# Performance work log

Measured on AMD Instinct MI355X. Metric: run time of the kernel, lower is better.

Reference implementation:

```python
import jax, jax.numpy as jnp
import numpy as np

N_NODES = 100000
N_RAND_EDGES = 6400000
N_EDGES = N_RAND_EDGES + N_NODES  # + self loops (dgl.add_self_loop)
IN_FEATS, HIDDEN, N_CLASSES = 16, 8, 2


def setup_inputs() -> dict:
    key = jax.random.key(0)
    ks = jax.random.split(key, 8)
    x = jax.random.normal(ks[0], (N_NODES, IN_FEATS), dtype=jnp.float32)
    src_r = jax.random.randint(ks[1], (N_RAND_EDGES,), 0, N_NODES, dtype=jnp.int32)
    dst_r = jax.random.randint(ks[2], (N_RAND_EDGES,), 0, N_NODES, dtype=jnp.int32)
    loop = jnp.arange(N_NODES, dtype=jnp.int32)
    src = jnp.concatenate([src_r, loop])
    dst = jnp.concatenate([dst_r, loop])
    timestamp = jax.random.uniform(ks[3], (N_EDGES,), dtype=jnp.float32)
    W1 = jax.random.normal(ks[4], (IN_FEATS, HIDDEN), dtype=jnp.float32) / np.sqrt(IN_FEATS)
    b1 = jnp.zeros((HIDDEN,), dtype=jnp.float32)
    W2 = jax.random.normal(ks[5], (HIDDEN, N_CLASSES), dtype=jnp.float32) / np.sqrt(HIDDEN)
    b2 = jnp.zeros((N_CLASSES,), dtype=jnp.float32)
    return {"x": x, "src": src, "dst": dst, "timestamp": timestamp,
            "W1": W1, "b1": b1, "W2": W2, "b2": b2}


def _gcn_layer(h, src, dst, ts, W, b):
    # message: u_mul_e -> src feature scaled by scalar edge weight  [E, F]
    msg = h[src] * ts[:, None]
    # reduce: max over incoming edges per destination node
    agg = jax.ops.segment_max(msg, dst, num_segments=N_NODES)
    # DGL fills nodes with no in-edges with 0 (self-loops make this rare)
    agg = jnp.where(jnp.isfinite(agg), agg, 0.0)
    return agg @ W + b


def reference(x, src, dst, timestamp, W1, b1, W2, b2):
    h = _gcn_layer(x, src, dst, timestamp, W1, b1)
    h = jax.nn.relu(h)
    # dropout(p=0.5, train=False) -> identity in eval mode
    out = _gcn_layer(h, src, dst, timestamp, W2, b2)
    return out
```

## Files before the change

kernel.cpp:

```cpp
#include <hip/hip_runtime.h>
#include <hip/hip_bf16.h>

#define N_NODES 100000
#define N_EDGES 6500000
#define IN_FEATS 16
#define HIDDEN 8
#define N_CLASSES 2
#define BK 196
#define NBK 512
#define EPB 8192
#define CAP 16384

__device__ __forceinline__ unsigned f2key(float f) {
    int i = __float_as_int(f);
    return (unsigned)(i ^ ((i >> 31) | 0x80000000));
}
__device__ __forceinline__ float key2f(unsigned u) {
    int i = (u & 0x80000000u) ? (int)(u ^ 0x80000000u) : (int)(~u);
    return __int_as_float(i);
}
__device__ __forceinline__ unsigned pack_bf16(float f0, float f1) {
    unsigned u0 = __float_as_uint(f0), u1 = __float_as_uint(f1);
    u0 = (u0 + 0x7FFFu + ((u0 >> 16) & 1u)) >> 16;
    u1 = (u1 + 0x7FFFu + ((u1 >> 16) & 1u)) >> 16;
    return u0 | (u1 << 16);
}

__global__ void init_cursor(unsigned* __restrict__ cursor) {
    int t = threadIdx.x;
    if (t < NBK) cursor[t] = (unsigned)t * CAP;
}

__global__ __launch_bounds__(1024, 8) void binfill(
    const float* __restrict__ x, const int* __restrict__ src,
    const int* __restrict__ dst, const float* __restrict__ ts,
    unsigned* __restrict__ cursor, uint2* __restrict__ binned,
    unsigned* __restrict__ xb) {
    __shared__ uint2 stage[EPB];
    __shared__ unsigned lcnt[NBK];
    __shared__ unsigned lstart[NBK + 1];
    __shared__ unsigned shiftv[NBK];
    __shared__ unsigned waveTot[8], waveBase[8];
    int t = threadIdx.x;
    if (t < NBK) lcnt[t] = 0u;
    for (int i = blockIdx.x * 1024 + t; i < N_NODES * IN_FEATS / 2; i += gridDim.x * 1024)
        xb[i] = pack_bf16(x[2 * i], x[2 * i + 1]);
    __syncthreads();
    int base = blockIdx.x * EPB;
    unsigned pk[8];
#pragma unroll
    for (int k = 0; k < 8; ++k) {
        int e = base + k * 1024 + t;
        pk[k] = 0xFFFFFFFFu;
        if (e < N_EDGES) {
            unsigned d = (unsigned)dst[e];
            unsigned b = d / BK;
            unsigned slot = atomicAdd(&lcnt[b], 1u);
            pk[k] = ((d - b * BK) << 22) | (b << 13) | slot;
        }
    }
    __syncthreads();
    unsigned c = (t < NBK) ? lcnt[t] : 0u;
    unsigned inc = c;
    int lane = t & 63;
#pragma unroll
    for (int d = 1; d < 64; d <<= 1) {
        unsigned v = __shfl_up(inc, d, 64);
        if (lane >= d) inc += v;
    }
    if (t < NBK && lane == 63) waveTot[t >> 6] = inc;
    __syncthreads();
    if (t == 0) {
        unsigned acc = 0;
#pragma unroll
        for (int w = 0; w < 8; ++w) { waveBase[w] = acc; acc += waveTot[w]; }
    }
    __syncthreads();
    if (t < NBK) {
        unsigned excl = waveBase[t >> 6] + inc - c;
        lstart[t] = excl;
        unsigned gb = atomicAdd(&cursor[t], c);
        shiftv[t] = gb - excl;
        if (t == NBK - 1) lstart[NBK] = excl + c;
    }
    __syncthreads();
#pragma unroll
    for (int k = 0; k < 8; ++k) {
        if (pk[k] != 0xFFFFFFFFu) {
            int e = base + k * 1024 + t;
            unsigned b = (pk[k] >> 13) & 511u;
            unsigned pos = lstart[b] + (pk[k] & 8191u);
            unsigned sv = (unsigned)__builtin_nontemporal_load(&src[e]);
            float tv = __builtin_nontemporal_load(&ts[e]);
            stage[pos] = make_uint2(sv | ((pk[k] >> 22) << 17), __float_as_uint(tv));
        }
    }
    __syncthreads();
    unsigned total = lstart[NBK];
#pragma unroll
    for (int j = 0; j < 8; ++j) {
        unsigned i = (unsigned)t + j * 1024u;
        if (i < total) {
            unsigned lo = 0, hi = NBK - 1;
            while (lo < hi) {
                unsigned mid = (lo + hi + 1) >> 1;
                if (lstart[mid] <= i) lo = mid; else hi = mid - 1;
            }
            uint2 v = stage[i];
            __builtin_nontemporal_store(((unsigned long long)v.y << 32) | v.x,
                                        (unsigned long long*)&binned[i + shiftv[lo]]);
        }
    }
}

__device__ __forceinline__ void agg16(unsigned* row, uint4 a, uint4 b, float tv) {
    const unsigned* pa = (const unsigned*)&a;
    const unsigned* pb = (const unsigned*)&b;
#pragma unroll
    for (int w = 0; w < 8; ++w) {
        unsigned u = (w < 4) ? pa[w] : pb[w - 4];
        atomicMax(row + 2 * w,     f2key(__uint_as_float(u << 16) * tv));
        atomicMax(row + 2 * w + 1, f2key(__uint_as_float(u & 0xFFFF0000u) * tv));
    }
}

__global__ __launch_bounds__(1024, 8) void layer1(
    const unsigned* __restrict__ cursor, const uint2* __restrict__ binned,
    const uint4* __restrict__ xb, const float* __restrict__ W1,
    const float* __restrict__ b1, uint4* __restrict__ hb) {
    __shared__ unsigned tile[BK * 17];
    __shared__ float sW[IN_FEATS * HIDDEN];
    __shared__ float sb[HIDDEN];
    int t = threadIdx.x;
    if (t < IN_FEATS * HIDDEN) sW[t] = W1[t];
    if (t < HIDDEN) sb[t] = b1[t];
    for (int i = t; i < BK * 17; i += 1024) tile[i] = 0u;
    __syncthreads();
    unsigned e0 = blockIdx.x * CAP;
    unsigned e1 = cursor[blockIdx.x];
    unsigned e = e0 + t;
    for (; e + 2048 < e1; e += 3072) {
        unsigned long long r0 = __builtin_nontemporal_load((const unsigned long long*)&binned[e]);
        unsigned long long r1 = __builtin_nontemporal_load((const unsigned long long*)&binned[e + 1024]);
        unsigned long long r2 = __builtin_nontemporal_load((const unsigned long long*)&binned[e + 2048]);
        unsigned s0 = (unsigned)r0 & 0x1FFFFu, d0 = ((unsigned)r0) >> 17;
        unsigned s1 = (unsigned)r1 & 0x1FFFFu, d1 = ((unsigned)r1) >> 17;
        unsigned s2 = (unsigned)r2 & 0x1FFFFu, d2 = ((unsigned)r2) >> 17;
        float t0 = __uint_as_float((unsigned)(r0 >> 32));
        float t1 = __uint_as_float((unsigned)(r1 >> 32));
        float t2 = __uint_as_float((unsigned)(r2 >> 32));
        uint4 a0 = xb[s0 * 2], c0 = xb[s0 * 2 + 1];
        uint4 a1 = xb[s1 * 2], c1 = xb[s1 * 2 + 1];
        uint4 a2 = xb[s2 * 2], c2 = xb[s2 * 2 + 1];
        agg16(tile + d0 * 17, a0, c0, t0);
        agg16(tile + d1 * 17, a1, c1, t1);
        agg16(tile + d2 * 17, a2, c2, t2);
    }
    for (; e < e1; e += 1024) {
        unsigned long long r0 = __builtin_nontemporal_load((const unsigned long long*)&binned[e]);
        unsigned s0 = (unsigned)r0 & 0x1FFFFu, d0 = ((unsigned)r0) >> 17;
        float t0 = __uint_as_float((unsigned)(r0 >> 32));
        uint4 a0 = xb[s0 * 2], c0 = xb[s0 * 2 + 1];
        agg16(tile + d0 * 17, a0, c0, t0);
    }
    __syncthreads();
    int node = blockIdx.x * BK + t;
    if (t < BK && node < N_NODES) {
        float a[IN_FEATS];
#pragma unroll
        for (int f = 0; f < IN_FEATS; ++f) a[f] = key2f(tile[t * 17 + f]);
        float o[HIDDEN];
#pragma unroll
        for (int j = 0; j < HIDDEN; ++j) {
            float sacc = sb[j];
#pragma unroll
            for (int f = 0; f < IN_FEATS; ++f) sacc += a[f] * sW[f * HIDDEN + j];
            o[j] = fmaxf(sacc, 0.f);
        }
        hb[node] = make_uint4(pack_bf16(o[0], o[1]), pack_bf16(o[2], o[3]),
                              pack_bf16(o[4], o[5]), pack_bf16(o[6], o[7]));
    }
}

__device__ __forceinline__ void agg8(unsigned* row, uint4 a, float tv) {
    const unsigned* pa = (const unsigned*)&a;
#pragma unroll
    for (int w = 0; w < 4; ++w) {
        unsigned u = pa[w];
        atomicMax(row + 2 * w,     f2key(__uint_as_float(u << 16) * tv));
        atomicMax(row + 2 * w + 1, f2key(__uint_as_float(u & 0xFFFF0000u) * tv));
    }
}

__global__ __launch_bounds__(1024, 8) void layer2(
    const unsigned* __restrict__ cursor, const uint2* __restrict__ binned,
    const uint4* __restrict__ hb, const float* __restrict__ W2,
    const float* __restrict__ b2, float* __restrict__ out) {
    __shared__ unsigned tile[BK * 9];
    __shared__ float sW[HIDDEN * N_CLASSES];
    __shared__ float sb[N_CLASSES];
    int t = threadIdx.x;
    if (t < HIDDEN * N_CLASSES) sW[t] = W2[t];
    if (t < N_CLASSES) sb[t] = b2[t];
    for (int i = t; i < BK * 9; i += 1024) tile[i] = 0u;
    __syncthreads();
    unsigned e0 = blockIdx.x * CAP;
    unsigned e1 = cursor[blockIdx.x];
    unsigned e = e0 + t;
    for (; e + 3072 < e1; e += 4096) {
        unsigned long long r0 = __builtin_nontemporal_load((const unsigned long long*)&binned[e]);
        unsigned long long r1 = __builtin_nontemporal_load((const unsigned long long*)&binned[e + 1024]);
        unsigned long long r2 = __builtin_nontemporal_load((const unsigned long long*)&binned[e + 2048]);
        unsigned long long r3 = __builtin_nontemporal_load((const unsigned long long*)&binned[e + 3072]);
        unsigned s0 = (unsigned)r0 & 0x1FFFFu, d0 = ((unsigned)r0) >> 17;
        unsigned s1 = (unsigned)r1 & 0x1FFFFu, d1 = ((unsigned)r1) >> 17;
        unsigned s2 = (unsigned)r2 & 0x1FFFFu, d2 = ((unsigned)r2) >> 17;
        unsigned s3 = (unsigned)r3 & 0x1FFFFu, d3 = ((unsigned)r3) >> 17;
        float t0 = __uint_as_float((unsigned)(r0 >> 32));
        float t1 = __uint_as_float((unsigned)(r1 >> 32));
        float t2 = __uint_as_float((unsigned)(r2 >> 32));
        float t3 = __uint_as_float((unsigned)(r3 >> 32));
        uint4 h0 = hb[s0], h1 = hb[s1], h2 = hb[s2], h3 = hb[s3];
        agg8(tile + d0 * 9, h0, t0);
        agg8(tile + d1 * 9, h1, t1);
        agg8(tile + d2 * 9, h2, t2);
        agg8(tile + d3 * 9, h3, t3);
    }
    for (; e < e1; e += 1024) {
        unsigned long long r0 = __builtin_nontemporal_load((const unsigned long long*)&binned[e]);
        unsigned s0 = (unsigned)r0 & 0x1FFFFu, d0 = ((unsigned)r0) >> 17;
        float t0 = __uint_as_float((unsigned)(r0 >> 32));
        agg8(tile + d0 * 9, hb[s0], t0);
    }
    __syncthreads();
    int node = blockIdx.x * BK + t;
    if (t < BK && node < N_NODES) {
        float a[HIDDEN];
#pragma unroll
        for (int f = 0; f < HIDDEN; ++f) a[f] = key2f(tile[t * 9 + f]);
        float o0 = sb[0], o1 = sb[1];
#pragma unroll
        for (int f = 0; f < HIDDEN; ++f) {
            o0 += a[f] * sW[f * N_CLASSES + 0];
            o1 += a[f] * sW[f * N_CLASSES + 1];
        }
        ((float2*)out)[node] = make_float2(o0, o1);
    }
}

__global__ void fb_init_keys(unsigned* __restrict__ k1, unsigned* __restrict__ k2) {
    int i = blockIdx.x * blockDim.x + threadIdx.x;
    for (int idx = i; idx < N_NODES * IN_FEATS; idx += gridDim.x * blockDim.x) k1[idx] = 0u;
    for (int idx = i; idx < N_NODES * HIDDEN; idx += gridDim.x * blockDim.x) k2[idx] = 0u;
}
__global__ void fb_scatter1(const int* __restrict__ src, const int* __restrict__ dst,
                            const float* __restrict__ ts, const float* __restrict__ x,
                            unsigned* __restrict__ agg) {
    int e = blockIdx.x * blockDim.x + threadIdx.x;
    if (e >= N_EDGES) return;
    int s = src[e]; int d = dst[e]; float t = ts[e];
    const float4* xs = (const float4*)(x + (size_t)s * IN_FEATS);
    unsigned* a = agg + (size_t)d * IN_FEATS;
#pragma unroll
    for (int q = 0; q < 4; ++q) {
        float4 v = xs[q];
        atomicMax(a + q * 4 + 0, f2key(v.x * t));
        atomicMax(a + q * 4 + 1, f2key(v.y * t));
        atomicMax(a + q * 4 + 2, f2key(v.z * t));
        atomicMax(a + q * 4 + 3, f2key(v.w * t));
    }
}
__global__ void fb_node1(const unsigned* __restrict__ agg, const float* __restrict__ W1,
                         const float* __restrict__ b1, float* __restrict__ h) {
    int n = blockIdx.x * blockDim.x + threadIdx.x;
    if (n >= N_NODES) return;
    float a[IN_FEATS];
#pragma unroll
    for (int f = 0; f < IN_FEATS; ++f) a[f] = key2f(agg[(size_t)n * IN_FEATS + f]);
#pragma unroll
    for (int j = 0; j < HIDDEN; ++j) {
        float acc = b1[j];
#pragma unroll
        for (int f = 0; f < IN_FEATS; ++f) acc += a[f] * W1[f * HIDDEN + j];
        h[(size_t)n * HIDDEN + j] = acc > 0.f ? acc : 0.f;
    }
}
__global__ void fb_scatter2(const int* __restrict__ src, const int* __restrict__ dst,
                            const float* __restrict__ ts, const float* __restrict__ h,
                            unsigned* __restrict__ agg) {
    int e = blockIdx.x * blockDim.x + threadIdx.x;
    if (e >= N_EDGES) return;
    int s = src[e]; int d = dst[e]; float t = ts[e];
    const float4* hs = (const float4*)(h + (size_t)s * HIDDEN);
    unsigned* a = agg + (size_t)d * HIDDEN;
#pragma unroll
    for (int q = 0; q < 2; ++q) {
        float4 v = hs[q];
        atomicMax(a + q * 4 + 0, f2key(v.x * t));
        atomicMax(a + q * 4 + 1, f2key(v.y * t));
        atomicMax(a + q * 4 + 2, f2key(v.z * t));
        atomicMax(a + q * 4 + 3, f2key(v.w * t));
    }
}
__global__ void fb_node2(const unsigned* __restrict__ agg, const float* __restrict__ W2,
                         const float* __restrict__ b2, float* __restrict__ out) {
    int n = blockIdx.x * blockDim.x + threadIdx.x;
    if (n >= N_NODES) return;
    float a[HIDDEN];
#pragma unroll
    for (int f = 0; f < HIDDEN; ++f) a[f] = key2f(agg[(size_t)n * HIDDEN + f]);
#pragma unroll
    for (int j = 0; j < N_CLASSES; ++j) {
        float acc = b2[j];
#pragma unroll
        for (int f = 0; f < HIDDEN; ++f) acc += a[f] * W2[f * N_CLASSES + j];
        out[(size_t)n * N_CLASSES + j] = acc;
    }
}

extern "C" void kernel_launch(void* const* d_in, const int* in_sizes, int n_in,
                              void* d_out, int out_size, void* d_ws, size_t ws_size,
                              hipStream_t stream) {
    const float* x  = (const float*)d_in[0];
    const int* src  = (const int*)d_in[1];
    const int* dst  = (const int*)d_in[2];
    const float* ts = (const float*)d_in[3];
    const float* W1 = (const float*)d_in[4];
    const float* b1 = (const float*)d_in[5];
    const float* W2 = (const float*)d_in[6];
    const float* b2 = (const float*)d_in[7];
    float* out = (float*)d_out;

    char* ws = (char*)d_ws;
    size_t off = 0;
    auto alloc = [&](size_t bytes) { char* p = ws + off; off += (bytes + 255) & ~(size_t)255; return p; };

    unsigned* cursor = (unsigned*)alloc(NBK * 4);
    uint2*    binned = (uint2*)alloc((size_t)NBK * CAP * 8);
    uint4*    hb     = (uint4*)alloc((size_t)N_NODES * 16);
    unsigned* xb     = (unsigned*)alloc((size_t)N_NODES * IN_FEATS * 2);
    size_t fast_need = off;

    int eblocks = (N_EDGES + EPB - 1) / EPB;

    if (fast_need <= ws_size) {
        init_cursor<<<1, NBK, 0, stream>>>(cursor);
        binfill<<<eblocks, 1024, 0, stream>>>(x, src, dst, ts, cursor, binned, xb);
        layer1<<<NBK, 1024, 0, stream>>>(cursor, binned, (const uint4*)xb, W1, b1, hb);
        layer2<<<NBK, 1024, 0, stream>>>(cursor, binned, hb, W2, b2, out);
    } else {
        unsigned* k1 = (unsigned*)d_ws;
        float* hh    = (float*)(k1 + (size_t)N_NODES * IN_FEATS);
        unsigned* k2 = (unsigned*)(hh + (size_t)N_NODES * HIDDEN);
        int eb = (N_EDGES + 255) / 256;
        fb_init_keys<<<2048, 256, 0, stream>>>(k1, k2);
        fb_scatter1<<<eb, 256, 0, stream>>>(src, dst, ts, x, k1);
        fb_node1<<<(N_NODES + 255) / 256, 256, 0, stream>>>(k1, W1, b1, hh);
        fb_scatter2<<<eb, 256, 0, stream>>>(src, dst, ts, hh, k2);
        fb_node2<<<(N_NODES + 255) / 256, 256, 0, stream>>>(k2, W2, b2, out);
    }
}
```

Before: 174.7 us.

## Skip redundant LDS atomics via read-check, batch dst loads, cheaper bin lookup

The aggregation kernels now read the current shared-memory max pair with one 64-bit load and issue atomicMax only when the new key is larger. This is meant to cut the LDS atomic traffic that dominates the segment-max. Tiles are padded to even strides (18 and 10 words) so the pair loads stay 8-byte aligned, at the cost of some bank conflicts. In binfill, dst loads are batched up front, and the per-element binary search is replaced by one search per 64-element chunk followed by a short linear scan.

```diff
diff --git a/kernel.cpp b/kernel.cpp
--- a/kernel.cpp
+++ b/kernel.cpp
@@ -40,6 +40,7 @@
     __shared__ unsigned lcnt[NBK];
     __shared__ unsigned lstart[NBK + 1];
     __shared__ unsigned shiftv[NBK];
+    __shared__ unsigned chunkb[EPB / 64];
     __shared__ unsigned waveTot[8], waveBase[8];
     int t = threadIdx.x;
     if (t < NBK) lcnt[t] = 0u;
@@ -47,13 +48,18 @@
         xb[i] = pack_bf16(x[2 * i], x[2 * i + 1]);
     __syncthreads();
     int base = blockIdx.x * EPB;
-    unsigned pk[8];
+    unsigned dvals[8];
 #pragma unroll
     for (int k = 0; k < 8; ++k) {
         int e = base + k * 1024 + t;
+        dvals[k] = (e < N_EDGES) ? (unsigned)__builtin_nontemporal_load(&dst[e]) : 0xFFFFFFFFu;
+    }
+    unsigned pk[8];
+#pragma unroll
+    for (int k = 0; k < 8; ++k) {
         pk[k] = 0xFFFFFFFFu;
-        if (e < N_EDGES) {
-            unsigned d = (unsigned)dst[e];
+        if (dvals[k] != 0xFFFFFFFFu) {
+            unsigned d = dvals[k];
             unsigned b = d / BK;
             unsigned slot = atomicAdd(&lcnt[b], 1u);
             pk[k] = ((d - b * BK) << 22) | (b << 13) | slot;
@@ -97,15 +103,24 @@
     }
     __syncthreads();
     unsigned total = lstart[NBK];
-#pragma unroll
-    for (int j = 0; j < 8; ++j) {
-        unsigned i = (unsigned)t + j * 1024u;
+    if (t < EPB / 64) {
+        unsigned i = (unsigned)t * 64u;
         if (i < total) {
             unsigned lo = 0, hi = NBK - 1;
             while (lo < hi) {
                 unsigned mid = (lo + hi + 1) >> 1;
                 if (lstart[mid] <= i) lo = mid; else hi = mid - 1;
             }
+            chunkb[t] = lo;
+        }
+    }
+    __syncthreads();
+#pragma unroll
+    for (int j = 0; j < 8; ++j) {
+        unsigned i = (unsigned)t + j * 1024u;
+        if (i < total) {
+            unsigned lo = chunkb[i >> 6];
+            while (i >= lstart[lo + 1]) ++lo;
             uint2 v = stage[i];
             __builtin_nontemporal_store(((unsigned long long)v.y << 32) | v.x,
                                         (unsigned long long*)&binned[i + shiftv[lo]]);
@@ -113,14 +128,17 @@
     }
 }
 
-__device__ __forceinline__ void agg16(unsigned* row, uint4 a, uint4 b, float tv) {
+__device__ __forceinline__ void agg16c(unsigned* row, uint4 a, uint4 b, float tv) {
     const unsigned* pa = (const unsigned*)&a;
     const unsigned* pb = (const unsigned*)&b;
 #pragma unroll
     for (int w = 0; w < 8; ++w) {
         unsigned u = (w < 4) ? pa[w] : pb[w - 4];
-        atomicMax(row + 2 * w,     f2key(__uint_as_float(u << 16) * tv));
-        atomicMax(row + 2 * w + 1, f2key(__uint_as_float(u & 0xFFFF0000u) * tv));
+        unsigned k0 = f2key(__uint_as_float(u << 16) * tv);
+        unsigned k1 = f2key(__uint_as_float(u & 0xFFFF0000u) * tv);
+        uint2 cur = *(const uint2*)(row + 2 * w);
+        if (k0 > cur.x) atomicMax(row + 2 * w,     k0);
+        if (k1 > cur.y) atomicMax(row + 2 * w + 1, k1);
     }
 }
 
@@ -128,13 +146,14 @@
     const unsigned* __restrict__ cursor, const uint2* __restrict__ binned,
     const uint4* __restrict__ xb, const float* __restrict__ W1,
     const float* __restrict__ b1, uint4* __restrict__ hb) {
-    __shared__ unsigned tile[BK * 17];
+    __shared__ uint2 tile2[BK * 9];
     __shared__ float sW[IN_FEATS * HIDDEN];
     __shared__ float sb[HIDDEN];
+    unsigned* tile = (unsigned*)tile2;
     int t = threadIdx.x;
     if (t < IN_FEATS * HIDDEN) sW[t] = W1[t];
     if (t < HIDDEN) sb[t] = b1[t];
-    for (int i = t; i < BK * 17; i += 1024) tile[i] = 0u;
+    for (int i = t; i < BK * 9; i += 1024) tile2[i] = make_uint2(0u, 0u);
     __syncthreads();
     unsigned e0 = blockIdx.x * CAP;
     unsigned e1 = cursor[blockIdx.x];
@@ -152,23 +171,23 @@
         uint4 a0 = xb[s0 * 2], c0 = xb[s0 * 2 + 1];
         uint4 a1 = xb[s1 * 2], c1 = xb[s1 * 2 + 1];
         uint4 a2 = xb[s2 * 2], c2 = xb[s2 * 2 + 1];
-        agg16(tile + d0 * 17, a0, c0, t0);
-        agg16(tile + d1 * 17, a1, c1, t1);
-        agg16(tile + d2 * 17, a2, c2, t2);
+        agg16c(tile + d0 * 18, a0, c0, t0);
+        agg16c(tile + d1 * 18, a1, c1, t1);
+        agg16c(tile + d2 * 18, a2, c2, t2);
     }
     for (; e < e1; e += 1024) {
         unsigned long long r0 = __builtin_nontemporal_load((const unsigned long long*)&binned[e]);
         unsigned s0 = (unsigned)r0 & 0x1FFFFu, d0 = ((unsigned)r0) >> 17;
         float t0 = __uint_as_float((unsigned)(r0 >> 32));
         uint4 a0 = xb[s0 * 2], c0 = xb[s0 * 2 + 1];
-        agg16(tile + d0 * 17, a0, c0, t0);
+        agg16c(tile + d0 * 18, a0, c0, t0);
     }
     __syncthreads();
     int node = blockIdx.x * BK + t;
     if (t < BK && node < N_NODES) {
         float a[IN_FEATS];
 #pragma unroll
-        for (int f = 0; f < IN_FEATS; ++f) a[f] = key2f(tile[t * 17 + f]);
+        for (int f = 0; f < IN_FEATS; ++f) a[f] = key2f(tile[t * 18 + f]);
         float o[HIDDEN];
 #pragma unroll
         for (int j = 0; j < HIDDEN; ++j) {
@@ -182,13 +201,16 @@
     }
 }
 
-__device__ __forceinline__ void agg8(unsigned* row, uint4 a, float tv) {
+__device__ __forceinline__ void agg8c(unsigned* row, uint4 a, float tv) {
     const unsigned* pa = (const unsigned*)&a;
 #pragma unroll
     for (int w = 0; w < 4; ++w) {
         unsigned u = pa[w];
-        atomicMax(row + 2 * w,     f2key(__uint_as_float(u << 16) * tv));
-        atomicMax(row + 2 * w + 1, f2key(__uint_as_float(u & 0xFFFF0000u) * tv));
+        unsigned k0 = f2key(__uint_as_float(u << 16) * tv);
+        unsigned k1 = f2key(__uint_as_float(u & 0xFFFF0000u) * tv);
+        uint2 cur = *(const uint2*)(row + 2 * w);
+        if (k0 > cur.x) atomicMax(row + 2 * w,     k0);
+        if (k1 > cur.y) atomicMax(row + 2 * w + 1, k1);
     }
 }
 
@@ -196,13 +218,14 @@
     const unsigned* __restrict__ cursor, const uint2* __restrict__ binned,
     const uint4* __restrict__ hb, const float* __restrict__ W2,
     const float* __restrict__ b2, float* __restrict__ out) {
-    __shared__ unsigned tile[BK * 9];
+    __shared__ uint2 tile2[BK * 5];
     __shared__ float sW[HIDDEN * N_CLASSES];
     __shared__ float sb[N_CLASSES];
+    unsigned* tile = (unsigned*)tile2;
     int t = threadIdx.x;
     if (t < HIDDEN * N_CLASSES) sW[t] = W2[t];
     if (t < N_CLASSES) sb[t] = b2[t];
-    for (int i = t; i < BK * 9; i += 1024) tile[i] = 0u;
+    for (int i = t; i < BK * 5; i += 1024) tile2[i] = make_uint2(0u, 0u);
     __syncthreads();
     unsigned e0 = blockIdx.x * CAP;
     unsigned e1 = cursor[blockIdx.x];
@@ -221,23 +244,23 @@
         float t2 = __uint_as_float((unsigned)(r2 >> 32));
         float t3 = __uint_as_float((unsigned)(r3 >> 32));
         uint4 h0 = hb[s0], h1 = hb[s1], h2 = hb[s2], h3 = hb[s3];
-        agg8(tile + d0 * 9, h0, t0);
-        agg8(tile + d1 * 9, h1, t1);
-        agg8(tile + d2 * 9, h2, t2);
-        agg8(tile + d3 * 9, h3, t3);
+        agg8c(tile + d0 * 10, h0, t0);
+        agg8c(tile + d1 * 10, h1, t1);
+        agg8c(tile + d2 * 10, h2, t2);
+        agg8c(tile + d3 * 10, h3, t3);
     }
     for (; e < e1; e += 1024) {
         unsigned long long r0 = __builtin_nontemporal_load((const unsigned long long*)&binned[e]);
         unsigned s0 = (unsigned)r0 & 0x1FFFFu, d0 = ((unsigned)r0) >> 17;
         float t0 = __uint_as_float((unsigned)(r0 >> 32));
-        agg8(tile + d0 * 9, hb[s0], t0);
+        agg8c(tile + d0 * 10, hb[s0], t0);
     }
     __syncthreads();
     int node = blockIdx.x * BK + t;
     if (t < BK && node < N_NODES) {
         float a[HIDDEN];
 #pragma unroll
-        for (int f = 0; f < HIDDEN; ++f) a[f] = key2f(tile[t * 9 + f]);
+        for (int f = 0; f < HIDDEN; ++f) a[f] = key2f(tile[t * 10 + f]);
         float o0 = sb[0], o1 = sb[1];
 #pragma unroll
         for (int f = 0; f < HIDDEN; ++f) {
```

After: 166.2 us. -4.8%, faster.
